# Performance work log

Measured on AMD Instinct MI355X. Metric: run time of the kernel, lower is better.

Reference implementation:

```python
import jax, jax.numpy as jnp
import numpy as np

VOCAB = 100000
EMBED = 300
HIDDEN = 300
BATCH = 32768
K_NEG = 10
N_CLASSES = 2
EPS = 1e-5
DENO_W = 1.0
CONO_W = 1.0


def setup_inputs() -> dict:
    key = jax.random.key(0)
    ks = jax.random.split(key, 12)
    init_range = 1.0 / EMBED
    return {
        "center_word_ids": jax.random.randint(ks[0], (BATCH,), 0, VOCAB),
        "context_word_ids": jax.random.randint(ks[1], (BATCH,), 0, VOCAB),
        "neg_context_ids": jax.random.randint(ks[2], (BATCH, K_NEG), 0, VOCAB),
        "party_label": jax.random.randint(ks[3], (BATCH,), 0, N_CLASSES),
        "center_emb": jax.random.uniform(ks[4], (VOCAB, EMBED), jnp.float32, -init_range, init_range),
        "context_emb": jax.random.normal(ks[5], (VOCAB, EMBED), jnp.float32) * 0.02,
        "W_enc": jax.random.normal(ks[6], (HIDDEN, EMBED), jnp.float32) * (1.0 / np.sqrt(EMBED)),
        "b_enc": jnp.zeros((HIDDEN,), jnp.float32),
        "W_dec": jax.random.normal(ks[7], (EMBED, HIDDEN), jnp.float32) * (1.0 / np.sqrt(HIDDEN)),
        "b_dec": jnp.zeros((EMBED,), jnp.float32),
        "W_cls": jax.random.normal(ks[8], (N_CLASSES, HIDDEN), jnp.float32) * (1.0 / np.sqrt(HIDDEN)),
        "b_cls": jnp.zeros((N_CLASSES,), jnp.float32),
    }


def reference(center_word_ids, context_word_ids, neg_context_ids, party_label,
              center_emb, context_emb, W_enc, b_enc, W_dec, b_dec, W_cls, b_cls):
    # encoder_forward (dropout p=0 -> identity)
    emb = center_emb[center_word_ids]                      # [B, E]
    enc = emb @ W_enc.T + b_enc                            # [B, H]
    # deno_forward: skip-gram negative sampling
    center_v = enc @ W_dec.T + b_dec                       # [B, E]
    ctx_v = context_emb[context_word_ids]                  # [B, E]
    pos_score = jnp.clip(jnp.sum(center_v * ctx_v, axis=1), -10.0, 10.0)
    pos = -jax.nn.log_sigmoid(pos_score)                   # [B]
    neg_v = context_emb[neg_context_ids]                   # [B, K, E]
    neg_score = jnp.clip(jnp.einsum('bke,be->bk', neg_v, center_v), -10.0, 10.0)
    neg = -jnp.sum(jax.nn.log_sigmoid(-neg_score), axis=1)  # [B]
    deno_loss = jnp.clip(jnp.mean(pos + neg), EPS, 10.0)
    # cono_forward + cross entropy
    logits = enc @ W_cls.T + b_cls                         # [B, C]
    logp = jax.nn.log_softmax(logits, axis=-1)
    nll = -jnp.take_along_axis(logp, party_label[:, None], axis=1)[:, 0]
    cono_loss = jnp.clip(jnp.mean(nll), EPS, 10.0)
    encoder_loss = jnp.clip(DENO_W * deno_loss + CONO_W * cono_loss, EPS, None)
    return jnp.stack([encoder_loss, deno_loss, cono_loss])
```

## Files before the change

### kernel.cpp

```cpp
#include <hip/hip_runtime.h>
#include <math.h>

#define VOCAB   100000
#define EMBED   300
#define HIDDEN  300
#define BATCH   32768
#define K_NEG   10
#define EPSV    1e-5f

#define KPAD      320
#define NPAD      384
#define CV_STRIDE 304
#define CTX8_STRIDE 304
#define WC2_STRIDE 304
#define FP8_SCALE 64.0f
#define FP8_DESCALE 0.015625f
#define NBUCKET 512

typedef __attribute__((ext_vector_type(8))) short  short8;
typedef __attribute__((ext_vector_type(4))) float  f32x4;
typedef __attribute__((ext_vector_type(2))) float  floatx2;

#if defined(__has_builtin)
#if __has_builtin(__builtin_amdgcn_cvt_pk_f32_fp8) && __has_builtin(__builtin_amdgcn_cvt_pk_fp8_f32)
#define HAVE_CVT_FP8 1
#endif
#endif

__device__ inline float b2f(unsigned short u) {
    union { unsigned int i; float f; } v; v.i = ((unsigned int)u) << 16; return v.f;
}
__device__ inline unsigned short f2b(float f) {
    union { float f; unsigned int i; } v; v.f = f;
    unsigned int r = v.i + 0x7FFFu + ((v.i >> 16) & 1u);
    return (unsigned short)(r >> 16);
}
__device__ inline void up2(unsigned int u, float& lo, float& hi) {
    union { unsigned int i; float f; } a, b;
    a.i = u << 16; b.i = u & 0xFFFF0000u;
    lo = a.f; hi = b.f;
}
__device__ inline float softplusf(float x) {
    return x > 0.f ? x + log1pf(expf(-x)) : log1pf(expf(x));
}

__device__ inline float fp8_to_f(unsigned int u8) {
    const unsigned s = (u8 >> 7) & 1, e = (u8 >> 3) & 15, m = u8 & 7;
    float v;
    if (e) { union { unsigned i; float f; } b; b.i = ((e + 120u) << 23) | (m << 20); v = b.f; }
    else v = (float)m * 0.001953125f;
    return s ? -v : v;
}
__device__ inline unsigned char f_to_fp8(float x) {
    union { float f; unsigned i; } b; b.f = x;
    const unsigned s = (b.i >> 31) << 7;
    const float a = fabsf(x);
    if (a >= 440.f) return (unsigned char)(s | 0x7E);
    if (a < 0.015625f) {
        int m = (int)rintf(a * 512.f);
        return (unsigned char)(m >= 8 ? (s | 0x08) : (s | (unsigned)m));
    }
    unsigned r = (b.i & 0x7FFFFFFFu) + 0x7FFFFu + ((b.i >> 20) & 1u);
    unsigned e8 = (r >> 23) - 120u;
    unsigned m8 = (r >> 20) & 7u;
    if (e8 > 15u) return (unsigned char)(s | 0x7E);
    return (unsigned char)(s | (e8 << 3) | m8);
}
__device__ inline unsigned enc4fp8(float a, float b, float c, float d) {
#ifdef HAVE_CVT_FP8
    int v = 0;
    v = __builtin_amdgcn_cvt_pk_fp8_f32(a, b, v, false);
    v = __builtin_amdgcn_cvt_pk_fp8_f32(c, d, v, true);
    return (unsigned)v;
#else
    return (unsigned)f_to_fp8(a) | ((unsigned)f_to_fp8(b) << 8) |
           ((unsigned)f_to_fp8(c) << 16) | ((unsigned)f_to_fp8(d) << 24);
#endif
}
__device__ inline void dec4fp8(unsigned u, float* f) {
#ifdef HAVE_CVT_FP8
    floatx2 lo = __builtin_amdgcn_cvt_pk_f32_fp8((int)u, false);
    floatx2 hi = __builtin_amdgcn_cvt_pk_f32_fp8((int)u, true);
    f[0] = lo[0]; f[1] = lo[1]; f[2] = hi[0]; f[3] = hi[1];
#else
    f[0] = fp8_to_f(u); f[1] = fp8_to_f(u >> 8);
    f[2] = fp8_to_f(u >> 16); f[3] = fp8_to_f(u >> 24);
#endif
}

__device__ inline void load_lds16(const void* g, void* l) {
    __builtin_amdgcn_global_load_lds(
        (const __attribute__((address_space(1))) unsigned int*)g,
        (__attribute__((address_space(3))) unsigned int*)l, 16, 0, 0);
}

#define NE (BATCH * 40)
#define NC (VOCAB * 19)

__global__ __launch_bounds__(256)
void prep_kernel(const float* __restrict__ cemb, const int* __restrict__ cids,
                 const float* __restrict__ xemb,
                 unsigned short* __restrict__ emb_b, unsigned char* __restrict__ ctx8)
{
    const int gid = blockIdx.x * 256 + threadIdx.x;
    if (gid < NE) {
        const int row = gid / 40;
        const int c8  = (gid - row * 40) * 8;
        const float* src = cemb + (size_t)cids[row] * 300;
        unsigned short t[8];
        if (c8 + 7 < 300) {
            float4 a = *(const float4*)(src + c8);
            float4 b = *(const float4*)(src + c8 + 4);
            t[0]=f2b(a.x); t[1]=f2b(a.y); t[2]=f2b(a.z); t[3]=f2b(a.w);
            t[4]=f2b(b.x); t[5]=f2b(b.y); t[6]=f2b(b.z); t[7]=f2b(b.w);
        } else {
            #pragma unroll
            for (int j = 0; j < 8; ++j) {
                const int c = c8 + j;
                t[j] = (c < 300) ? f2b(src[c]) : (unsigned short)0;
            }
        }
        *(uint4*)(emb_b + (size_t)row * KPAD + c8) = *(const uint4*)t;
    } else if (gid < NE + NC) {
        const int g3  = gid - NE;
        const int row = g3 / 19;
        const int l   = g3 - row * 19;
        const int e0  = l * 16;
        const float* src = xemb + (size_t)row * 300 + e0;
        float v[16];
        #pragma unroll
        for (int q = 0; q < 4; ++q) {
            if (e0 + q * 4 + 3 < 300) {
                float4 a = *(const float4*)(src + q * 4);
                v[q*4+0]=a.x; v[q*4+1]=a.y; v[q*4+2]=a.z; v[q*4+3]=a.w;
            } else {
                #pragma unroll
                for (int j = 0; j < 4; ++j) {
                    const int e = e0 + q * 4 + j;
                    v[q*4+j] = (e < 300) ? src[q*4+j] : 0.f;
                }
            }
        }
        unsigned u[4];
        #pragma unroll
        for (int q = 0; q < 4; ++q)
            u[q] = enc4fp8(v[q*4]*FP8_SCALE, v[q*4+1]*FP8_SCALE,
                           v[q*4+2]*FP8_SCALE, v[q*4+3]*FP8_SCALE);
        *(uint4*)(ctx8 + (size_t)row * CTX8_STRIDE + e0) = make_uint4(u[0],u[1],u[2],u[3]);
    }
}

__global__ __launch_bounds__(256)
void w2_kernel(const float* __restrict__ Wd, const float* __restrict__ We,
               unsigned short* __restrict__ w2p)
{
    __shared__ float ds[16][33];
    __shared__ float es[32][17];
    const int tid = threadIdx.x;
    const int tn = tid >> 4, tk = tid & 15;
    const int n = blockIdx.y * 16 + tn;
    const int k = blockIdx.x * 16 + tk;

    float acc = 0.f;
    for (int h0 = 0; h0 < 300; h0 += 32) {
        {
            const int i = tid * 2;
            const int a = i >> 5, h = i & 31;
            const int rr = blockIdx.y * 16 + a;
            #pragma unroll
            for (int j = 0; j < 2; ++j) {
                const int hh = h + j;
                ds[a][hh] = (rr < 300 && h0 + hh < 300) ? Wd[rr * 300 + h0 + hh] : 0.f;
            }
        }
        {
            const int i = tid * 2;
            const int h = i >> 4, c = i & 15;
            const int cc = blockIdx.x * 16 + c;
            #pragma unroll
            for (int j = 0; j < 2; ++j)
                es[h][c + j] = (h0 + h < 300 && cc + j < 300) ? We[(h0 + h) * 300 + cc + j] : 0.f;
        }
        __syncthreads();
        #pragma unroll
        for (int h = 0; h < 32; ++h)
            acc = fmaf(ds[tn][h], es[h][tk], acc);
        __syncthreads();
    }
    if (n < NPAD && k < KPAD)
        w2p[n * KPAD + k] = (n < 300 && k < 300) ? f2b(acc) : (unsigned short)0;
}

__global__ __launch_bounds__(320)
void wb_kernel(const float* __restrict__ Wd, const float* __restrict__ We,
               const float* __restrict__ Wc, const float* __restrict__ b_enc,
               const float* __restrict__ b_dec, const float* __restrict__ b_cls,
               float* __restrict__ wc2, float* __restrict__ bias2, float* __restrict__ bc2)
{
    const int c = threadIdx.x;
    if (c < WC2_STRIDE) {
        float b2 = 0.f, a0 = 0.f, a1 = 0.f;
        if (c < 300) {
            for (int k = 0; k < 300; ++k) b2 = fmaf(Wd[c * 300 + k], b_enc[k], b2);
            for (int h = 0; h < 300; ++h) {
                const float we = We[h * 300 + c];
                a0 = fmaf(Wc[h], we, a0);
                a1 = fmaf(Wc[300 + h], we, a1);
            }
            b2 += b_dec[c];
        }
        bias2[c] = b2;
        wc2[c] = a0;
        wc2[WC2_STRIDE + c] = a1;
    } else if (c < WC2_STRIDE + 2) {
        const int j = c - WC2_STRIDE;
        float s = 0.f;
        for (int h = 0; h < 300; ++h) s = fmaf(Wc[j * 300 + h], b_enc[h], s);
        bc2[j] = s + b_cls[j];
    }
}

__global__ __launch_bounds__(256)
void gemm_cv_kernel(const unsigned short* __restrict__ A,
                    const unsigned short* __restrict__ B,
                    const float* __restrict__ bias,
                    unsigned short* __restrict__ C)
{
    __shared__ unsigned short As[2][128 * 32];
    __shared__ unsigned short Bs[2][128 * 32];

    const int tid  = threadIdx.x;
    const int wave = tid >> 6;
    const int lane = tid & 63;
    const int m0 = blockIdx.y * 128;
    const int n0 = blockIdx.x * 128;

    const int wr = (wave & 1) * 64;
    const int wc = (wave >> 1) * 64;
    const int fr = lane & 15;
    const int fq = lane >> 4;

    const unsigned short* gA[2];
    const unsigned short* gB[2];
    int ldsOff[2];
    #pragma unroll
    for (int inst = 0; inst < 2; ++inst) {
        const int t = wave * 2 + inst;
        const int r = (t << 4) + (lane >> 2);
        const int c = ((lane & 3) - r - (r >> 2)) & 3;
        gA[inst] = A + (size_t)(m0 + r) * KPAD + c * 8;
        gB[inst] = B + (size_t)(n0 + r) * KPAD + c * 8;
        ldsOff[inst] = t << 9;
    }

    int aoff[4], boff[4];
    #pragma unroll
    for (int i = 0; i < 4; ++i) {
        const int ra = wr + i * 16 + fr;
        aoff[i] = (ra << 5) + (((fq + ra + (ra >> 2)) & 3) << 3);
        const int rb = wc + i * 16 + fr;
        boff[i] = (rb << 5) + (((fq + rb + (rb >> 2)) & 3) << 3);
    }

    f32x4 acc[4][4] = {};

    #pragma unroll
    for (int inst = 0; inst < 2; ++inst) {
        load_lds16(gA[inst], &As[0][ldsOff[inst]]);
        load_lds16(gB[inst], &Bs[0][ldsOff[inst]]);
    }

    int cur = 0;
    for (int ki = 0; ki < KPAD / 32; ++ki) {
        __syncthreads();
        if (ki + 1 < KPAD / 32) {
            const int k0 = (ki + 1) * 32;
            #pragma unroll
            for (int inst = 0; inst < 2; ++inst) {
                load_lds16(gA[inst] + k0, &As[cur ^ 1][ldsOff[inst]]);
                load_lds16(gB[inst] + k0, &Bs[cur ^ 1][ldsOff[inst]]);
            }
        }
        short8 af[4], bf[4];
        #pragma unroll
        for (int i = 0; i < 4; ++i) af[i] = *(const short8*)&As[cur][aoff[i]];
        #pragma unroll
        for (int j = 0; j < 4; ++j) bf[j] = *(const short8*)&Bs[cur][boff[j]];
        #pragma unroll
        for (int i = 0; i < 4; ++i)
            #pragma unroll
            for (int j = 0; j < 4; ++j)
                acc[i][j] = __builtin_amdgcn_mfma_f32_16x16x32_bf16(
                    af[i], bf[j], acc[i][j], 0, 0, 0);
        cur ^= 1;
    }

    #pragma unroll
    for (int i = 0; i < 4; ++i) {
        #pragma unroll
        for (int r = 0; r < 4; ++r) {
            const int m = m0 + wr + i * 16 + fq * 4 + r;
            unsigned short* crow = C + (size_t)m * CV_STRIDE;
            #pragma unroll
            for (int j = 0; j < 4; ++j) {
                const int n = n0 + wc + j * 16 + fr;
                if (n < 300) {
                    crow[n] = f2b(acc[i][j][r] + bias[n]);
                } else if (n < CV_STRIDE) {
                    crow[n] = 0;
                }
            }
        }
    }
}

__global__ __launch_bounds__(256)
void score_kernel(const unsigned short* __restrict__ cvb,
                  const unsigned char* __restrict__ ctx8,
                  const int* __restrict__ ctx_ids, const int* __restrict__ neg_ids,
                  float* __restrict__ db)
{
    const int wid  = threadIdx.x >> 6;
    const int lane = threadIdx.x & 63;
    const int l5   = lane & 31;
    const int unit = blockIdx.x * 8 + wid * 2 + (lane >> 5);
    const int row  = unit / 3;
    const int g    = unit - row * 3;
    const bool act = l5 < 19;

    const int b = row * K_NEG;
    int ids[4]; bool inc[4]; bool pos[4];
    #pragma unroll
    for (int j = 0; j < 4; ++j) {
        const int t = g * 4 - 1 + j;
        pos[j] = (t < 0);
        inc[j] = (t <= 9);
        ids[j] = pos[j] ? ctx_ids[row] : neg_ids[b + (t > 9 ? 9 : t)];
    }

    const uint4 Z4 = make_uint4(0, 0, 0, 0);
    const char* cvp = (const char*)(cvb + (size_t)row * CV_STRIDE);
    uint4 c0 = act ? *(const uint4*)(cvp + l5 * 32)      : Z4;
    uint4 c1 = act ? *(const uint4*)(cvp + l5 * 32 + 16) : Z4;

    uint4 gv[4];
    #pragma unroll
    for (int j = 0; j < 4; ++j)
        gv[j] = act ? *(const uint4*)(ctx8 + (size_t)ids[j] * CTX8_STRIDE + l5 * 16) : Z4;

    float cvf[16];
    up2(c0.x, cvf[0], cvf[1]);  up2(c0.y, cvf[2], cvf[3]);
    up2(c0.z, cvf[4], cvf[5]);  up2(c0.w, cvf[6], cvf[7]);
    up2(c1.x, cvf[8], cvf[9]);  up2(c1.y, cvf[10], cvf[11]);
    up2(c1.z, cvf[12], cvf[13]);up2(c1.w, cvf[14], cvf[15]);

    float ds[4];
    #pragma unroll
    for (int j = 0; j < 4; ++j) {
        float gf[16];
        dec4fp8(gv[j].x, gf); dec4fp8(gv[j].y, gf + 4);
        dec4fp8(gv[j].z, gf + 8); dec4fp8(gv[j].w, gf + 12);
        float s = 0.f;
        #pragma unroll
        for (int e = 0; e < 16; ++e) s = fmaf(cvf[e], gf[e], s);
        ds[j] = s;
    }
    #pragma unroll
    for (int j = 0; j < 4; ++j) {
        float v = ds[j];
        #pragma unroll
        for (int m = 16; m; m >>= 1) v += __shfl_xor(v, m);
        ds[j] = v;
    }

    if (l5 == 0) {
        float local = 0.f;
        #pragma unroll
        for (int j = 0; j < 4; ++j) {
            if (inc[j]) {
                float s = fminf(10.f, fmaxf(-10.f, ds[j] * FP8_DESCALE));
                local += softplusf(pos[j] ? -s : s);
            }
        }
        atomicAdd(&db[blockIdx.x & (NBUCKET - 1)], local);
    }
}

__global__ __launch_bounds__(256)
void ce_kernel(const unsigned short* __restrict__ embb,
               const int* __restrict__ labels,
               const float* __restrict__ wc2, const float* __restrict__ bc2,
               float* __restrict__ cb)
{
    const int wid  = threadIdx.x >> 6;
    const int lane = threadIdx.x & 63;
    const int l5   = lane & 31;
    const int row  = blockIdx.x * 8 + wid * 2 + (lane >> 5);
    const bool act = l5 < 19;

    const uint4 Z4 = make_uint4(0, 0, 0, 0);
    const char* evp = (const char*)(embb + (size_t)row * KPAD);
    uint4 e0 = act ? *(const uint4*)(evp + l5 * 32)      : Z4;
    uint4 e1 = act ? *(const uint4*)(evp + l5 * 32 + 16) : Z4;
    float ev[16];
    up2(e0.x, ev[0], ev[1]);  up2(e0.y, ev[2], ev[3]);
    up2(e0.z, ev[4], ev[5]);  up2(e0.w, ev[6], ev[7]);
    up2(e1.x, ev[8], ev[9]);  up2(e1.y, ev[10], ev[11]);
    up2(e1.z, ev[12], ev[13]);up2(e1.w, ev[14], ev[15]);

    float p0 = 0.f, p1 = 0.f;
    if (act) {
        const float* w0 = wc2 + l5 * 16;
        const float* w1 = wc2 + WC2_STRIDE + l5 * 16;
        #pragma unroll
        for (int q = 0; q < 4; ++q) {
            float4 a = *(const float4*)(w0 + q * 4);
            float4 c = *(const float4*)(w1 + q * 4);
            p0 = fmaf(ev[q*4], a.x, p0); p0 = fmaf(ev[q*4+1], a.y, p0);
            p0 = fmaf(ev[q*4+2], a.z, p0); p0 = fmaf(ev[q*4+3], a.w, p0);
            p1 = fmaf(ev[q*4], c.x, p1); p1 = fmaf(ev[q*4+1], c.y, p1);
            p1 = fmaf(ev[q*4+2], c.z, p1); p1 = fmaf(ev[q*4+3], c.w, p1);
        }
    }
    #pragma unroll
    for (int m = 16; m; m >>= 1) { p0 += __shfl_xor(p0, m); p1 += __shfl_xor(p1, m); }

    if (l5 == 0) {
        const float l0 = p0 + bc2[0];
        const float l1 = p1 + bc2[1];
        const float mx = fmaxf(l0, l1);
        const float lse = mx + logf(expf(l0 - mx) + expf(l1 - mx));
        const float nll = lse - (labels[row] ? l1 : l0);
        atomicAdd(&cb[blockIdx.x & (NBUCKET - 1)], nll);
    }
}

__device__ inline float wave_red64(float v) {
    #pragma unroll
    for (int o = 32; o; o >>= 1) v += __shfl_down(v, o);
    return v;
}
__global__ __launch_bounds__(256)
void finalize_kernel(const float* __restrict__ db, const float* __restrict__ cb,
                     float* __restrict__ out)
{
    const int t = threadIdx.x;
    float d = db[t] + db[t + 256];
    float c = cb[t] + cb[t + 256];
    d = wave_red64(d); c = wave_red64(c);
    __shared__ float sd[4], sc[4];
    if ((t & 63) == 0) { sd[t >> 6] = d; sc[t >> 6] = c; }
    __syncthreads();
    if (t == 0) {
        const float inv = 1.0f / (float)BATCH;
        float deno = (sd[0] + sd[1] + sd[2] + sd[3]) * inv;
        float cono = (sc[0] + sc[1] + sc[2] + sc[3]) * inv;
        deno = fminf(10.f, fmaxf(EPSV, deno));
        cono = fminf(10.f, fmaxf(EPSV, cono));
        out[0] = fmaxf(EPSV, deno + cono);
        out[1] = deno;
        out[2] = cono;
    }
}

extern "C" void kernel_launch(void* const* d_in, const int* in_sizes, int n_in,
                              void* d_out, int out_size, void* d_ws, size_t ws_size,
                              hipStream_t stream)
{
    const int*   cids  = (const int*)d_in[0];
    const int*   ctx   = (const int*)d_in[1];
    const int*   neg   = (const int*)d_in[2];
    const int*   lab   = (const int*)d_in[3];
    const float* cemb  = (const float*)d_in[4];
    const float* xemb  = (const float*)d_in[5];
    const float* W_enc = (const float*)d_in[6];
    const float* b_enc = (const float*)d_in[7];
    const float* W_dec = (const float*)d_in[8];
    const float* b_dec = (const float*)d_in[9];
    const float* W_cls = (const float*)d_in[10];
    const float* b_cls = (const float*)d_in[11];
    float* out = (float*)d_out;

    unsigned short* emb_b = (unsigned short*)d_ws;
    unsigned short* cv_b  = emb_b + (size_t)BATCH * KPAD;
    unsigned char*  ctx8  = (unsigned char*)(cv_b + (size_t)BATCH * CV_STRIDE);
    unsigned short* w2p   = (unsigned short*)(ctx8 + (size_t)VOCAB * CTX8_STRIDE);
    float* wc2   = (float*)(w2p + (size_t)NPAD * KPAD);
    float* bias2 = wc2 + 2 * WC2_STRIDE;
    float* bc2   = bias2 + WC2_STRIDE;
    float* db    = bc2 + 4;
    float* cb    = db + NBUCKET;

    hipMemsetAsync(db, 0, 2 * NBUCKET * sizeof(float), stream);

    prep_kernel<<<(NE + NC + 255) / 256, 256, 0, stream>>>(cemb, cids, xemb, emb_b, ctx8);

    dim3 wgrid(KPAD / 16, NPAD / 16);
    w2_kernel<<<wgrid, 256, 0, stream>>>(W_dec, W_enc, w2p);
    wb_kernel<<<1, 320, 0, stream>>>(W_dec, W_enc, W_cls, b_enc, b_dec, b_cls,
                                     wc2, bias2, bc2);

    dim3 ggrid(3, BATCH / 128);
    gemm_cv_kernel<<<ggrid, 256, 0, stream>>>(emb_b, w2p, bias2, cv_b);

    score_kernel<<<3 * BATCH / 8, 256, 0, stream>>>(cv_b, ctx8, ctx, neg, db);
    ce_kernel<<<BATCH / 8, 256, 0, stream>>>(emb_b, lab, wc2, bc2, cb);

    finalize_kernel<<<1, 256, 0, stream>>>(db, cb, out);
}
```

Before: 423.4 us.

## Compute SGNS scores with bf16 MFMA and parallelize bias-weight precompute

The score kernel is restructured so that each wave handles 16 batch rows. The fp8 context rows are decoded to bf16 and multiplied against center vectors with 16x16x32 MFMA instructions, and only the diagonal entries of each 16x16 result are kept as scores. This replaces the per-lane scalar dot products and the shuffle reductions for each score. The single-block wb_kernel becomes 229 blocks with one wave per output reduction, and softplus now uses hardware exp2/log intrinsics. The MFMA path computes 16x more products than it needs, and the decoded fp8 values are rounded to bf16, which adds a small accuracy risk.

New measurement: 354.6 us. 16.3% less time.

```diff
diff --git a/kernel.cpp b/kernel.cpp
--- a/kernel.cpp
+++ b/kernel.cpp
@@ -40,8 +40,10 @@
     a.i = u << 16; b.i = u & 0xFFFF0000u;
     lo = a.f; hi = b.f;
 }
-__device__ inline float softplusf(float x) {
-    return x > 0.f ? x + log1pf(expf(-x)) : log1pf(expf(x));
+__device__ inline float softplus_fast(float x) {
+    const float t = __builtin_amdgcn_exp2f(fabsf(x) * -1.44269504f);
+    const float l = __builtin_amdgcn_logf(1.f + t) * 0.69314718f;
+    return fmaxf(x, 0.f) + l;
 }
 
 __device__ inline float fp8_to_f(unsigned int u8) {
@@ -92,6 +94,17 @@
     __builtin_amdgcn_global_load_lds(
         (const __attribute__((address_space(1))) unsigned int*)g,
         (__attribute__((address_space(3))) unsigned int*)l, 16, 0, 0);
+}
+
+__device__ inline float red64(float v) {
+    #pragma unroll
+    for (int m = 32; m; m >>= 1) v += __shfl_xor(v, m);
+    return v;
+}
+
+__device__ inline unsigned packbf2(float lo, float hi) {
+    union { float f; unsigned i; } a, b; a.f = lo; b.f = hi;
+    return (b.i & 0xFFFF0000u) | (a.i >> 16);
 }
 
 #define NE (BATCH * 40)
@@ -191,32 +204,35 @@
         w2p[n * KPAD + k] = (n < 300 && k < 300) ? f2b(acc) : (unsigned short)0;
 }
 
-__global__ __launch_bounds__(320)
+__global__ __launch_bounds__(256)
 void wb_kernel(const float* __restrict__ Wd, const float* __restrict__ We,
                const float* __restrict__ Wc, const float* __restrict__ b_enc,
                const float* __restrict__ b_dec, const float* __restrict__ b_cls,
                float* __restrict__ wc2, float* __restrict__ bias2, float* __restrict__ bc2)
 {
-    const int c = threadIdx.x;
-    if (c < WC2_STRIDE) {
-        float b2 = 0.f, a0 = 0.f, a1 = 0.f;
-        if (c < 300) {
-            for (int k = 0; k < 300; ++k) b2 = fmaf(Wd[c * 300 + k], b_enc[k], b2);
-            for (int h = 0; h < 300; ++h) {
-                const float we = We[h * 300 + c];
-                a0 = fmaf(Wc[h], we, a0);
-                a1 = fmaf(Wc[300 + h], we, a1);
-            }
-            b2 += b_dec[c];
-        }
-        bias2[c] = b2;
-        wc2[c] = a0;
-        wc2[WC2_STRIDE + c] = a1;
-    } else if (c < WC2_STRIDE + 2) {
-        const int j = c - WC2_STRIDE;
-        float s = 0.f;
-        for (int h = 0; h < 300; ++h) s = fmaf(Wc[j * 300 + h], b_enc[h], s);
-        bc2[j] = s + b_cls[j];
+    const int unit = blockIdx.x * 4 + (threadIdx.x >> 6);
+    const int lane = threadIdx.x & 63;
+    if (unit >= 914) return;
+    float s = 0.f;
+    if (unit < 304) {
+        const int c = unit;
+        if (c < 300)
+            for (int k = lane; k < 300; k += 64) s = fmaf(Wd[c * 300 + k], b_enc[k], s);
+        s = red64(s);
+        if (lane == 0) bias2[c] = (c < 300) ? s + b_dec[c] : 0.f;
+    } else if (unit < 912) {
+        const int u2 = unit - 304;
+        const int j = u2 >= 304 ? 1 : 0;
+        const int c = u2 - j * 304;
+        if (c < 300)
+            for (int h = lane; h < 300; h += 64) s = fmaf(Wc[j * 300 + h], We[h * 300 + c], s);
+        s = red64(s);
+        if (lane == 0) wc2[j * WC2_STRIDE + c] = s;
+    } else {
+        const int j = unit - 912;
+        for (int h = lane; h < 300; h += 64) s = fmaf(Wc[j * 300 + h], b_enc[h], s);
+        s = red64(s);
+        if (lane == 0) bc2[j] = s + b_cls[j];
     }
 }
 
@@ -322,68 +338,59 @@
 {
     const int wid  = threadIdx.x >> 6;
     const int lane = threadIdx.x & 63;
-    const int l5   = lane & 31;
-    const int unit = blockIdx.x * 8 + wid * 2 + (lane >> 5);
-    const int row  = unit / 3;
-    const int g    = unit - row * 3;
-    const bool act = l5 < 19;
-
-    const int b = row * K_NEG;
-    int ids[4]; bool inc[4]; bool pos[4];
-    #pragma unroll
-    for (int j = 0; j < 4; ++j) {
-        const int t = g * 4 - 1 + j;
-        pos[j] = (t < 0);
-        inc[j] = (t <= 9);
-        ids[j] = pos[j] ? ctx_ids[row] : neg_ids[b + (t > 9 ? 9 : t)];
-    }
-
-    const uint4 Z4 = make_uint4(0, 0, 0, 0);
-    const char* cvp = (const char*)(cvb + (size_t)row * CV_STRIDE);
-    uint4 c0 = act ? *(const uint4*)(cvp + l5 * 32)      : Z4;
-    uint4 c1 = act ? *(const uint4*)(cvp + l5 * 32 + 16) : Z4;
-
-    uint4 gv[4];
-    #pragma unroll
-    for (int j = 0; j < 4; ++j)
-        gv[j] = act ? *(const uint4*)(ctx8 + (size_t)ids[j] * CTX8_STRIDE + l5 * 16) : Z4;
-
-    float cvf[16];
-    up2(c0.x, cvf[0], cvf[1]);  up2(c0.y, cvf[2], cvf[3]);
-    up2(c0.z, cvf[4], cvf[5]);  up2(c0.w, cvf[6], cvf[7]);
-    up2(c1.x, cvf[8], cvf[9]);  up2(c1.y, cvf[10], cvf[11]);
-    up2(c1.z, cvf[12], cvf[13]);up2(c1.w, cvf[14], cvf[15]);
-
-    float ds[4];
-    #pragma unroll
-    for (int j = 0; j < 4; ++j) {
-        float gf[16];
-        dec4fp8(gv[j].x, gf); dec4fp8(gv[j].y, gf + 4);
-        dec4fp8(gv[j].z, gf + 8); dec4fp8(gv[j].w, gf + 12);
-        float s = 0.f;
-        #pragma unroll
-        for (int e = 0; e < 16; ++e) s = fmaf(cvf[e], gf[e], s);
-        ds[j] = s;
-    }
-    #pragma unroll
-    for (int j = 0; j < 4; ++j) {
-        float v = ds[j];
-        #pragma unroll
-        for (int m = 16; m; m >>= 1) v += __shfl_xor(v, m);
-        ds[j] = v;
-    }
-
-    if (l5 == 0) {
-        float local = 0.f;
-        #pragma unroll
-        for (int j = 0; j < 4; ++j) {
-            if (inc[j]) {
-                float s = fminf(10.f, fmaxf(-10.f, ds[j] * FP8_DESCALE));
-                local += softplusf(pos[j] ? -s : s);
-            }
-        }
-        atomicAdd(&db[blockIdx.x & (NBUCKET - 1)], local);
-    }
+    const int fr = lane & 15;
+    const int fq = lane >> 4;
+    const int r0 = (blockIdx.x * 4 + wid) * 16;
+    const int myrow = r0 + fr;
+
+    union { uint4 u; short8 v; } z16; z16.u = make_uint4(0, 0, 0, 0);
+
+    short8 af[10];
+    const unsigned short* arow = cvb + (size_t)myrow * CV_STRIDE + fq * 8;
+    #pragma unroll
+    for (int kk = 0; kk < 10; ++kk) {
+        if (kk < 9 || fq < 2) af[kk] = *(const short8*)(arow + kk * 32);
+        else af[kk] = z16.v;
+    }
+
+    int ids[11];
+    ids[0] = ctx_ids[myrow];
+    #pragma unroll
+    for (int j = 0; j < 10; ++j) ids[j + 1] = neg_ids[myrow * K_NEG + j];
+
+    const bool dlane = (fr >> 2) == fq;
+    const int  dreg  = fr & 3;
+    float loss = 0.f;
+
+    #pragma unroll
+    for (int j = 0; j < 11; ++j) {
+        const unsigned char* brow = ctx8 + (size_t)ids[j] * CTX8_STRIDE + fq * 8;
+        f32x4 acc = {};
+        #pragma unroll
+        for (int kk = 0; kk < 10; ++kk) {
+            uint2 u;
+            if (kk < 9 || fq < 2) u = *(const uint2*)(brow + kk * 32);
+            else u = make_uint2(0, 0);
+            float f[8];
+            dec4fp8(u.x, f); dec4fp8(u.y, f + 4);
+            union { unsigned w[4]; short8 v; } bf;
+            bf.w[0] = packbf2(f[0], f[1]);
+            bf.w[1] = packbf2(f[2], f[3]);
+            bf.w[2] = packbf2(f[4], f[5]);
+            bf.w[3] = packbf2(f[6], f[7]);
+            acc = __builtin_amdgcn_mfma_f32_16x16x32_bf16(af[kk], bf.v, acc, 0, 0, 0);
+        }
+        if (dlane) {
+            float dv = (dreg & 2) ? ((dreg & 1) ? acc[3] : acc[2])
+                                  : ((dreg & 1) ? acc[1] : acc[0]);
+            float s = dv * FP8_DESCALE;
+            s = fminf(10.f, fmaxf(-10.f, s));
+            loss += softplus_fast(j == 0 ? -s : s);
+        }
+    }
+
+    float v = red64(loss);
+    if (lane == 0) atomicAdd(&db[blockIdx.x & (NBUCKET - 1)], v);
 }
 
 __global__ __launch_bounds__(256)
@@ -497,13 +504,13 @@
 
     dim3 wgrid(KPAD / 16, NPAD / 16);
     w2_kernel<<<wgrid, 256, 0, stream>>>(W_dec, W_enc, w2p);
-    wb_kernel<<<1, 320, 0, stream>>>(W_dec, W_enc, W_cls, b_enc, b_dec, b_cls,
-                                     wc2, bias2, bc2);
+    wb_kernel<<<229, 256, 0, stream>>>(W_dec, W_enc, W_cls, b_enc, b_dec, b_cls,
+                                       wc2, bias2, bc2);
 
     dim3 ggrid(3, BATCH / 128);
     gemm_cv_kernel<<<ggrid, 256, 0, stream>>>(emb_b, w2p, bias2, cv_b);
 
-    score_kernel<<<3 * BATCH / 8, 256, 0, stream>>>(cv_b, ctx8, ctx, neg, db);
+    score_kernel<<<BATCH / 64, 256, 0, stream>>>(cv_b, ctx8, ctx, neg, db);
     ce_kernel<<<BATCH / 8, 256, 0, stream>>>(emb_b, lab, wc2, bc2, cb);
 
     finalize_kernel<<<1, 256, 0, stream>>>(db, cb, out);
```
